# Performance work log

Measured on AMD Instinct MI355X. Metric: run time of the kernel, lower is better.

Reference implementation:

```python
import jax, jax.numpy as jnp
import numpy as np

B, C, H, W = 2, 64, 128, 128
O = 64
KH = KW = 3
KK = KH * KW
STRIDE, PAD, DIL = 1, 1, 1
DG = 1            # deformable groups
CG = C // DG      # channels per deformable group
Ho = (H + 2 * PAD - DIL * (KH - 1) - 1) // STRIDE + 1
Wo = (W + 2 * PAD - DIL * (KW - 1) - 1) // STRIDE + 1


def setup_inputs() -> dict:
    key = jax.random.key(0)
    k1, k2, k3, k4, k5, k6 = jax.random.split(key, 6)
    input_offset = jax.random.normal(k1, (B, C, H, W), jnp.float32)
    input_real = jax.random.normal(k2, (B, C, H, W), jnp.float32)
    # conv_offset_mask: out = DG*3*KK channels. (Zero-init in the module; use
    # small random weights so offsets are non-trivial but only a few pixels.)
    w_om = jax.random.normal(k3, (DG * 3 * KK, C, KH, KW), jnp.float32) * 0.02
    b_om = jax.random.normal(k4, (DG * 3 * KK,), jnp.float32) * 0.02
    # DCN weight (groups=1): (O, C, KH, KW)
    fan_in = C * KK
    w_dcn = jax.random.normal(k5, (O, C, KH, KW), jnp.float32) / np.sqrt(fan_in)
    b_dcn = jax.random.normal(k6, (O,), jnp.float32) * 0.01
    return {"input_offset": input_offset, "input_real": input_real,
            "w_om": w_om, "b_om": b_om, "w_dcn": w_dcn, "b_dcn": b_dcn}


def _modulated_deform_conv(x, offset, mask, w, b):
    # x: (B,C,H,W); offset: (B, DG*2*KK, Ho, Wo) interleaved (y,x) per kernel pt
    # mask: (B, DG*KK, Ho, Wo) already sigmoid'ed; w: (O,C,KH,KW); b: (O,)
    off = offset.reshape(B, DG, KK, 2, Ho, Wo)
    off_y, off_x = off[:, :, :, 0], off[:, :, :, 1]          # (B,DG,KK,Ho,Wo)
    m = mask.reshape(B, DG, KK, Ho, Wo)

    ky = jnp.repeat(jnp.arange(KH), KW).astype(jnp.float32)  # (KK,)
    kx = jnp.tile(jnp.arange(KW), KH).astype(jnp.float32)
    base_y = (ky[:, None, None] * DIL
              + jnp.arange(Ho, dtype=jnp.float32)[None, :, None] * STRIDE - PAD)
    base_x = (kx[:, None, None] * DIL
              + jnp.arange(Wo, dtype=jnp.float32)[None, None, :] * STRIDE - PAD)
    y = base_y[None, None] + off_y                           # (B,DG,KK,Ho,Wo)
    x_ = base_x[None, None] + off_x

    y0 = jnp.floor(y); x0 = jnp.floor(x_)
    ly = y - y0; lx = x_ - x0
    hy = 1.0 - ly; hx = 1.0 - lx

    xg = x.reshape(B, DG, CG, H * W)                         # grouped spatialflat

    def gather(iy, ix):
        valid = ((iy >= 0) & (iy < H) & (ix >= 0) & (ix < W)).astype(jnp.float32)
        iyc = jnp.clip(iy, 0, H - 1).astype(jnp.int32)
        ixc = jnp.clip(ix, 0, W - 1).astype(jnp.int32)
        idx = (iyc * W + ixc).reshape(B, DG, 1, KK * Ho * Wo)
        v = jnp.take_along_axis(xg, idx, axis=3)
        v = v.reshape(B, DG, CG, KK, Ho, Wo)
        return v * valid[:, :, None]

    val = (gather(y0,       x0      ) * (hy * hx)[:, :, None]
         + gather(y0,       x0 + 1.0) * (hy * lx)[:, :, None]
         + gather(y0 + 1.0, x0      ) * (ly * hx)[:, :, None]
         + gather(y0 + 1.0, x0 + 1.0) * (ly * lx)[:, :, None])
    val = val * m[:, :, None]                                # (B,DG,CG,KK,Ho,Wo)

    wr = w.reshape(O, DG, CG, KK)
    out = jnp.einsum('bdckhw,odck->bohw', val, wr) + b[None, :, None, None]
    return out


def reference(input_offset, input_real, w_om, b_om, w_dcn, b_dcn):
    # conv_offset_mask
    om = jax.lax.conv_general_dilated(
        input_offset, w_om, window_strides=(STRIDE, STRIDE),
        padding=((PAD, PAD), (PAD, PAD)),
        dimension_numbers=('NCHW', 'OIHW', 'NCHW'))
    om = om + b_om[None, :, None, None]
    n = DG * KK
    o1, o2, mraw = om[:, :n], om[:, n:2 * n], om[:, 2 * n:]
    offset = jnp.concatenate((o1, o2), axis=1)               # (B, 2*DG*KK, Ho, Wo)
    mask = jax.nn.sigmoid(mraw)                              # (B, DG*KK, Ho, Wo)
    out = _modulated_deform_conv(input_real, offset, mask, w_dcn, b_dcn)
    return out, offset
```

## Files before the change

### kernel.cpp

```cpp
#include <hip/hip_runtime.h>
#include <math.h>

constexpr int BB   = 2;
constexpr int CC   = 64;
constexpr int HH   = 128;
constexpr int WW   = 128;
constexpr int OO   = 64;
constexpr int HWSZ = HH * WW;
constexpr int HOWO = 16384;
constexpr int OMC  = 27;

typedef __attribute__((ext_vector_type(8))) short short8v;
typedef __attribute__((ext_vector_type(4))) float f32x4;
typedef unsigned short ushortT;

__device__ __forceinline__ ushortT f2bf(float x) {
    unsigned int u = __builtin_bit_cast(unsigned int, x);
    u = (u + 0x7FFFu + ((u >> 16) & 1u)) >> 16;
    return (ushortT)u;
}
__device__ __forceinline__ float bf2f(ushortT u) {
    return __builtin_bit_cast(float, (unsigned int)u << 16);
}

__global__ __launch_bounds__(256) void xtpose_prep(
    const float* __restrict__ xr, const float* __restrict__ xo,
    ushortT* __restrict__ xtr, ushortT* __restrict__ xto,
    const float* __restrict__ w_dcn, const float* __restrict__ w_om,
    ushortT* __restrict__ Wdswz, ushortT* __restrict__ Womswz)
{
    __shared__ float t[64][129];
    const int tid = threadIdx.x;
    const int bid = blockIdx.x;

    if (bid < 512) {
        const int by = bid & 255;
        const int b  = by >> 7, y = by & 127;
        const float* src = (bid < 256) ? xr : xo;
        ushortT*    dst  = (bid < 256) ? xtr : xto;

#pragma unroll
        for (int cc = 0; cc < 64; cc += 2) {
            const int c  = cc + (tid >> 7);
            const int xw = tid & 127;
            t[c][xw] = src[((size_t)(b * 64 + c) * 128 + y) * 128 + xw];
        }
        __syncthreads();

#pragma unroll
        for (int r = 0; r < 8; ++r) {
            const int idx = r * 256 + tid;
            const int xw  = idx >> 4;
            const int cq  = (idx & 15) << 2;
            ushort4 pk = make_ushort4(f2bf(t[cq][xw]), f2bf(t[cq + 1][xw]),
                                      f2bf(t[cq + 2][xw]), f2bf(t[cq + 3][xw]));
            *(ushort4*)(dst + (((size_t)by * 128 + xw) << 6) + cq) = pk;
        }
    } else {
        const int idx = (bid - 512) * 256 + tid;
        if (idx < 64 * 576) {
            const int j    = idx & 7;
            const int lane = (idx >> 3) & 63;
            const int ks   = (idx >> 9) % 18;
            const int wid  = idx / (8 * 64 * 18);
            const int l15  = lane & 15;
            const int l4   = lane >> 4;
            const int oc   = (wid << 4) + l15;
            const int k    = ks * 32 + l4 * 8 + j;
            const int kk   = k >> 6;
            const int c    = k & 63;
            Wdswz[idx] = f2bf(w_dcn[(oc * CC + c) * 9 + kk]);
        }
        if (idx < 32 * 576) {
            const int j    = idx & 7;
            const int lane = (idx >> 3) & 63;
            const int ks   = (idx >> 9) % 18;
            const int half = idx / (8 * 64 * 18);
            const int l15  = lane & 15;
            const int l4   = lane >> 4;
            const int oc   = (half << 4) + l15;
            const int k    = ks * 32 + l4 * 8 + j;
            const int kk   = k >> 6;
            const int c    = k & 63;
            Womswz[idx] = (oc < OMC) ? f2bf(w_om[(oc * CC + c) * 9 + kk])
                                     : (ushortT)0;
        }
    }
}

__device__ __forceinline__ void bilinear_params(
    float oy, float ox, float m, int ho, int wo, int ky, int kx,
    float& w00, float& w01, float& w10, float& w11,
    int& i00, int& i01, int& i10, int& i11)
{
    const float yf = (float)(ho + ky - 1) + oy;
    const float xf = (float)(wo + kx - 1) + ox;
    const float y0 = floorf(yf), x0 = floorf(xf);
    const float ly = yf - y0, lx = xf - x0;
    const float hy = 1.f - ly, hx = 1.f - lx;
    const int iy0 = (int)y0, ix0 = (int)x0;
    const int iy1 = iy0 + 1, ix1 = ix0 + 1;
    const bool vy0 = (unsigned)iy0 < (unsigned)HH;
    const bool vy1 = (unsigned)iy1 < (unsigned)HH;
    const bool vx0 = (unsigned)ix0 < (unsigned)WW;
    const bool vx1 = (unsigned)ix1 < (unsigned)WW;
    w00 = (vy0 && vx0) ? hy * hx * m : 0.f;
    w01 = (vy0 && vx1) ? hy * lx * m : 0.f;
    w10 = (vy1 && vx0) ? ly * hx * m : 0.f;
    w11 = (vy1 && vx1) ? ly * lx * m : 0.f;
    const int cy0 = min(max(iy0, 0), HH - 1), cy1 = min(max(iy1, 0), HH - 1);
    const int cx0 = min(max(ix0, 0), WW - 1), cx1 = min(max(ix1, 0), WW - 1);
    i00 = cy0 * WW + cx0; i01 = cy0 * WW + cx1;
    i10 = cy1 * WW + cx0; i11 = cy1 * WW + cx1;
}

__device__ __forceinline__ void gather_issue(
    const int s, const int tid, const int pl, const size_t bbase,
    const float (*offm)[28], const ushortT* __restrict__ xtr,
    short8v (&pay)[3][4], float (&gw)[3][4], int (&wadr)[3])
{
    const int ch0 = (tid & 7) << 3;
#pragma unroll
    for (int rr = 0; rr < 3; ++rr) {
        const int rnd  = s * 3 + rr;
        const int task = rnd * 32 + (tid >> 3);
        const int gpix = task & 63;
        const int kk   = task >> 6;
        const int pg   = pl + gpix;
        const int gho  = pg >> 7, gwo = pg & 127;
        const int ky   = kk / 3, kx = kk - 3 * ky;

        float w00, w01, w10, w11; int i00, i01, i10, i11;
        bilinear_params(offm[gpix][2 * kk], offm[gpix][2 * kk + 1],
                        offm[gpix][18 + kk], gho, gwo, ky, kx,
                        w00, w01, w10, w11, i00, i01, i10, i11);
        gw[rr][0] = w00; gw[rr][1] = w01; gw[rr][2] = w10; gw[rr][3] = w11;

        pay[rr][0] = *(const short8v*)(xtr + ((bbase + i00) << 6) + ch0);
        pay[rr][1] = *(const short8v*)(xtr + ((bbase + i01) << 6) + ch0);
        pay[rr][2] = *(const short8v*)(xtr + ((bbase + i10) << 6) + ch0);
        pay[rr][3] = *(const short8v*)(xtr + ((bbase + i11) << 6) + ch0);

        wadr[rr] = gpix * 1152 + ((((kk << 6) + ch0) << 1) ^ ((gpix & 7) << 4));
    }
}

__device__ __forceinline__ void gather_combine(
    ushortT* vlds, const short8v (&pay)[3][4], const float (&gw)[3][4],
    const int (&wadr)[3])
{
#pragma unroll
    for (int rr = 0; rr < 3; ++rr) {
        short8v pk;
#pragma unroll
        for (int j = 0; j < 8; ++j) {
            const float v = gw[rr][0] * bf2f((ushortT)pay[rr][0][j]) +
                            gw[rr][1] * bf2f((ushortT)pay[rr][1][j]) +
                            gw[rr][2] * bf2f((ushortT)pay[rr][2][j]) +
                            gw[rr][3] * bf2f((ushortT)pay[rr][3][j]);
            pk[j] = (short)f2bf(v);
        }
        *(short8v*)((char*)vlds + wadr[rr]) = pk;
    }
}

__global__ __launch_bounds__(256, 2) void fused_mlp(
    const ushortT* __restrict__ xtr,
    const ushortT* __restrict__ xto,
    const ushortT* __restrict__ Womswz,
    const float* __restrict__ bom,
    const ushortT* __restrict__ Wdswz,
    const float* __restrict__ bd,
    float* __restrict__ out,
    float* __restrict__ off_out)
{
    __shared__ ushortT vlds[64 * 576];
    __shared__ float offm[64][28];

    const int tid  = threadIdx.x;
    const int lane = tid & 63;
    const int wid  = tid >> 6;
    const int l15  = lane & 15;
    const int l4   = lane >> 4;
    const int p0   = blockIdx.x * 64;
    const int b    = p0 >> 14;
    const int pl   = p0 & 16383;
    const size_t bbase = (size_t)(b << 14);

    {
        const int lpix = (wid << 4) + l15;
        const int pix  = pl + lpix;
        const int ho   = pix >> 7, wo = pix & 127;

        short8v xv[18];
        unsigned int vmask = 0;
#pragma unroll
        for (int ks = 0; ks < 18; ++ks) {
            const int kk = ks >> 1;
            const int ky = kk / 3, kx = kk - 3 * ky;
            const int iy = ho + ky - 1, ix = wo + kx - 1;
            if (((unsigned)iy < 128u) && ((unsigned)ix < 128u)) vmask |= (1u << ks);
            const int cy = min(max(iy, 0), 127), cx = min(max(ix, 0), 127);
            const int c0 = ((ks & 1) << 5) + (l4 << 3);
            xv[ks] = *(const short8v*)(xto + ((bbase + cy * 128 + cx) << 6) + c0);
        }

        f32x4 acc0 = {0.f, 0.f, 0.f, 0.f};
        f32x4 acc1 = {0.f, 0.f, 0.f, 0.f};
        const short8v zero8 = {0, 0, 0, 0, 0, 0, 0, 0};
        const ushortT* womL = Womswz + (lane << 3);

#pragma unroll
        for (int ks = 0; ks < 18; ++ks) {
            const short8v bf = (vmask & (1u << ks)) ? xv[ks] : zero8;
            const short8v ah0 = *(const short8v*)(womL + (ks << 9));
            const short8v ah1 = *(const short8v*)(womL + ((18 + ks) << 9));
            acc0 = __builtin_amdgcn_mfma_f32_16x16x32_bf16(ah0, bf, acc0, 0, 0, 0);
            acc1 = __builtin_amdgcn_mfma_f32_16x16x32_bf16(ah1, bf, acc1, 0, 0, 0);
        }

#pragma unroll
        for (int r = 0; r < 4; ++r) {
            const int oca = (l4 << 2) + r;
            const float va = acc0[r] + bom[oca];
            offm[lpix][oca] = va;
            off_out[(b * 18 + oca) * HOWO + pix] = va;
            const int ocb = 16 + (l4 << 2) + r;
            if (ocb < 18) {
                const float vb = acc1[r] + bom[ocb];
                offm[lpix][ocb] = vb;
                off_out[(b * 18 + ocb) * HOWO + pix] = vb;
            } else if (ocb < OMC) {
                offm[lpix][ocb] = 1.f / (1.f + expf(-(acc1[r] + bom[ocb])));
            }
        }
    }
    __syncthreads();

    {
        short8v payA[3][4], payB[3][4];
        float gwA[3][4], gwB[3][4];
        int wA[3], wB[3];

        gather_issue(0, tid, pl, bbase, offm, xtr, payA, gwA, wA);
        gather_issue(1, tid, pl, bbase, offm, xtr, payB, gwB, wB);
        gather_combine(vlds, payA, gwA, wA);
        gather_issue(2, tid, pl, bbase, offm, xtr, payA, gwA, wA);
        gather_combine(vlds, payB, gwB, wB);
        gather_issue(3, tid, pl, bbase, offm, xtr, payB, gwB, wB);
        gather_combine(vlds, payA, gwA, wA);
        gather_issue(4, tid, pl, bbase, offm, xtr, payA, gwA, wA);
        gather_combine(vlds, payB, gwB, wB);
        gather_issue(5, tid, pl, bbase, offm, xtr, payB, gwB, wB);
        gather_combine(vlds, payA, gwA, wA);
        gather_combine(vlds, payB, gwB, wB);
    }
    __syncthreads();

    {
        const int oc0 = wid << 4;
        const ushortT* wdL = Wdswz + ((wid * 18) << 9) + (lane << 3);
        const int swz = (l15 & 7) << 4;
        const int kl  = l4 << 4;

        f32x4 ac0 = {0.f, 0.f, 0.f, 0.f};
        f32x4 ac1 = {0.f, 0.f, 0.f, 0.f};
        f32x4 ac2 = {0.f, 0.f, 0.f, 0.f};
        f32x4 ac3 = {0.f, 0.f, 0.f, 0.f};

#pragma unroll
        for (int ks = 0; ks < 18; ++ks) {
            const short8v ahi = *(const short8v*)(wdL + (ks << 9));
            const int inrow = ((ks << 6) + kl) ^ swz;
            const char* base = (const char*)vlds + inrow;
            const short8v b0 = *(const short8v*)(base + (l15 + 0)  * 1152);
            const short8v b1 = *(const short8v*)(base + (l15 + 16) * 1152);
            const short8v b2 = *(const short8v*)(base + (l15 + 32) * 1152);
            const short8v b3 = *(const short8v*)(base + (l15 + 48) * 1152);
            ac0 = __builtin_amdgcn_mfma_f32_16x16x32_bf16(ahi, b0, ac0, 0, 0, 0);
            ac1 = __builtin_amdgcn_mfma_f32_16x16x32_bf16(ahi, b1, ac1, 0, 0, 0);
            ac2 = __builtin_amdgcn_mfma_f32_16x16x32_bf16(ahi, b2, ac2, 0, 0, 0);
            ac3 = __builtin_amdgcn_mfma_f32_16x16x32_bf16(ahi, b3, ac3, 0, 0, 0);
        }

#pragma unroll
        for (int r = 0; r < 4; ++r) {
            const int oc = oc0 + (l4 << 2) + r;
            const float bias = bd[oc];
            const size_t ob = ((size_t)(b * OO + oc)) * HOWO + pl + l15;
            out[ob + 0]  = ac0[r] + bias;
            out[ob + 16] = ac1[r] + bias;
            out[ob + 32] = ac2[r] + bias;
            out[ob + 48] = ac3[r] + bias;
        }
    }
}

__global__ __launch_bounds__(256) void prep_transpose(
    const float* __restrict__ w_dcn, const float* __restrict__ w_om,
    float* __restrict__ wt_dcn, float* __restrict__ wt_om)
{
    int idx = blockIdx.x * 256 + threadIdx.x;
    if (idx < 9 * 64 * 64) {
        int o  = idx & 63;
        int c  = (idx >> 6) & 63;
        int kk = idx >> 12;
        wt_dcn[idx] = w_dcn[(o * CC + c) * 9 + kk];
    }
    if (idx < 9 * 64 * 28) {
        int o    = idx % 28;
        int rest = idx / 28;
        int c    = rest & 63;
        int kk   = rest >> 6;
        wt_om[idx] = (o < OMC) ? w_om[(o * CC + c) * 9 + kk] : 0.f;
    }
}

__global__ __launch_bounds__(256) void conv_om2(
    const float* __restrict__ x, const float* __restrict__ wtom,
    const float* __restrict__ bom, float* __restrict__ off_out,
    float* __restrict__ mask_out)
{
    const int pg  = blockIdx.x * 256 + threadIdx.x;
    const int b   = pg >> 14;
    const int p   = pg & 16383;
    const int ho  = p >> 7, wo = p & 127;
    const int oc0 = blockIdx.y << 3;

    float acc[8];
#pragma unroll
    for (int j = 0; j < 8; ++j) acc[j] = 0.f;

    const float* xb = x + (size_t)b * CC * HWSZ;
    for (int c = 0; c < CC; ++c) {
        const float* xc = xb + c * HWSZ;
        float t[9];
#pragma unroll
        for (int kh = 0; kh < 3; ++kh) {
            const int ih = ho + kh - 1;
            const bool rv = (unsigned)ih < (unsigned)HH;
#pragma unroll
            for (int kw = 0; kw < 3; ++kw) {
                const int iw = wo + kw - 1;
                t[kh * 3 + kw] =
                    (rv && (unsigned)iw < (unsigned)WW) ? xc[ih * WW + iw] : 0.f;
            }
        }
#pragma unroll
        for (int kk = 0; kk < 9; ++kk) {
            const float tv = t[kk];
            const float4* wr = (const float4*)(wtom + ((kk << 6) + c) * 28 + oc0);
            const float4 w0 = wr[0];
            const float4 w1 = wr[1];
            acc[0] += tv * w0.x; acc[1] += tv * w0.y;
            acc[2] += tv * w0.z; acc[3] += tv * w0.w;
            acc[4] += tv * w1.x; acc[5] += tv * w1.y;
            acc[6] += tv * w1.z; acc[7] += tv * w1.w;
        }
    }
#pragma unroll
    for (int j = 0; j < 8; ++j) {
        const int oc = oc0 + j;
        if (oc < 18) {
            off_out[(b * 18 + oc) * HOWO + p] = acc[j] + bom[oc];
        } else if (oc < OMC) {
            mask_out[(b * 9 + (oc - 18)) * HOWO + p] =
                1.f / (1.f + expf(-(acc[j] + bom[oc])));
        }
    }
}

__global__ __launch_bounds__(256) void dcn2(
    const float* __restrict__ xr, const float* __restrict__ off,
    const float* __restrict__ mask, const float* __restrict__ wtd,
    const float* __restrict__ bd, float* __restrict__ out)
{
    __shared__ float offm[32][29];
    __shared__ float vtile[64 * 33];

    const int tid  = threadIdx.x;
    const int pixl = tid & 31;
    const int grp  = tid >> 5;
    const int p0g  = blockIdx.x * 32;
    const int b    = p0g >> 14;
    const int p0   = p0g & 16383;
    const int p    = p0 + pixl;
    const int ho   = p >> 7, wo = p & 127;

    for (int it = tid; it < 32 * 27; it += 256) {
        const int pp = it & 31;
        const int o  = it >> 5;
        offm[pp][o] = (o < 18)
            ? off[(b * 18 + o) * HOWO + p0 + pp]
            : mask[(b * 9 + (o - 18)) * HOWO + p0 + pp];
    }
    __syncthreads();

    float acc[8];
#pragma unroll
    for (int j = 0; j < 8; ++j) acc[j] = 0.f;

    const float* xrb = xr + (size_t)b * CC * HWSZ;

    for (int kk = 0; kk < 9; ++kk) {
        {
            const int ky = kk / 3, kx = kk - ky * 3;
            float w00, w01, w10, w11; int i00, i01, i10, i11;
            bilinear_params(offm[pixl][2 * kk], offm[pixl][2 * kk + 1],
                            offm[pixl][18 + kk], ho, wo, ky, kx,
                            w00, w01, w10, w11, i00, i01, i10, i11);
            const float* xg = xrb + (grp << 3) * HWSZ;
#pragma unroll
            for (int i = 0; i < 8; ++i) {
                const float* xc = xg + i * HWSZ;
                const float v = w00 * xc[i00] + w01 * xc[i01] +
                                w10 * xc[i10] + w11 * xc[i11];
                vtile[((grp << 3) + i) * 33 + pixl] = v;
            }
        }
        __syncthreads();

        const float* wk = wtd + (kk << 12) + (grp << 3);
#pragma unroll 8
        for (int c = 0; c < 64; ++c) {
            const float v = vtile[c * 33 + pixl];
            const float4* wr = (const float4*)(wk + (c << 6));
            const float4 w0 = wr[0];
            const float4 w1 = wr[1];
            acc[0] += v * w0.x; acc[1] += v * w0.y;
            acc[2] += v * w0.z; acc[3] += v * w0.w;
            acc[4] += v * w1.x; acc[5] += v * w1.y;
            acc[6] += v * w1.z; acc[7] += v * w1.w;
        }
        __syncthreads();
    }

#pragma unroll
    for (int q = 0; q < 8; ++q) {
        const int oc = (grp << 3) + q;
        out[((size_t)(b * OO + oc)) * HOWO + p0 + pixl] = acc[q] + bd[oc];
    }
}

__global__ __launch_bounds__(256) void conv_om_slow(
    const float* __restrict__ x, const float* __restrict__ w,
    const float* __restrict__ bias, float* __restrict__ off_out)
{
    const int xid = blockIdx.x;
    const int b   = xid >> 6;
    const int p   = ((xid & 63) << 8) + threadIdx.x;
    const int ho  = p >> 7, wo = p & 127;
    const int oc0 = blockIdx.y << 4;

    float acc[16];
#pragma unroll
    for (int j = 0; j < 16; ++j) {
        const int oc = oc0 + j;
        acc[j] = (oc < OMC) ? bias[oc] : 0.f;
    }
    const float* xb = x + (size_t)b * CC * HWSZ;
    for (int c = 0; c < CC; ++c) {
        const float* xc = xb + c * HWSZ;
        float t[9];
#pragma unroll
        for (int kh = 0; kh < 3; ++kh) {
            const int ih = ho + kh - 1;
            const bool rv = (unsigned)ih < (unsigned)HH;
#pragma unroll
            for (int kw = 0; kw < 3; ++kw) {
                const int iw = wo + kw - 1;
                t[kh * 3 + kw] =
                    (rv && (unsigned)iw < (unsigned)WW) ? xc[ih * WW + iw] : 0.f;
            }
        }
#pragma unroll
        for (int j = 0; j < 16; ++j) {
            const int oc = oc0 + j;
            if (oc < OMC) {
                const float* wj = w + (size_t)(oc * CC + c) * 9;
                float s = 0.f;
#pragma unroll
                for (int kk = 0; kk < 9; ++kk) s += t[kk] * wj[kk];
                acc[j] += s;
            }
        }
    }
#pragma unroll
    for (int j = 0; j < 16; ++j) {
        const int oc = oc0 + j;
        if (oc < 18) off_out[(b * 18 + oc) * HOWO + p] = acc[j];
    }
}

__global__ __launch_bounds__(256) void dcn_slow(
    const float* __restrict__ xr, const float* __restrict__ off,
    const float* __restrict__ wd, const float* __restrict__ bd,
    float* __restrict__ out, const float* __restrict__ xo,
    const float* __restrict__ wom, const float* __restrict__ bom)
{
    const int xid = blockIdx.x;
    const int b   = xid >> 6;
    const int p   = ((xid & 63) << 8) + threadIdx.x;
    const int ho  = p >> 7, wo = p & 127;
    const int o0  = blockIdx.y << 4;

    float acc[16];
#pragma unroll
    for (int j = 0; j < 16; ++j) acc[j] = bd[o0 + j];
    const float* xb = xr + (size_t)b * CC * HWSZ;

    for (int kk = 0; kk < 9; ++kk) {
        const float oy = off[(b * 18 + 2 * kk) * HOWO + p];
        const float ox = off[(b * 18 + 2 * kk + 1) * HOWO + p];
        float a = bom[18 + kk];
        const float* xob = xo + (size_t)b * CC * HWSZ;
        for (int c = 0; c < CC; ++c) {
            const float* xc2 = xob + c * HWSZ;
            const float* wj  = wom + (size_t)((18 + kk) * CC + c) * 9;
#pragma unroll
            for (int kh = 0; kh < 3; ++kh) {
                const int ih = ho + kh - 1;
                if ((unsigned)ih < (unsigned)HH) {
#pragma unroll
                    for (int kw = 0; kw < 3; ++kw) {
                        const int iw = wo + kw - 1;
                        if ((unsigned)iw < (unsigned)WW)
                            a += xc2[ih * WW + iw] * wj[kh * 3 + kw];
                    }
                }
            }
        }
        const float m = 1.f / (1.f + expf(-a));
        const int ky = kk / 3, kx = kk - ky * 3;
        float w00, w01, w10, w11; int i00, i01, i10, i11;
        bilinear_params(oy, ox, m, ho, wo, ky, kx,
                        w00, w01, w10, w11, i00, i01, i10, i11);
#pragma unroll 4
        for (int c = 0; c < CC; ++c) {
            const float* xc = xb + c * HWSZ;
            const float v = w00 * xc[i00] + w01 * xc[i01] +
                            w10 * xc[i10] + w11 * xc[i11];
#pragma unroll
            for (int j = 0; j < 16; ++j)
                acc[j] += v * wd[(size_t)((o0 + j) * CC + c) * 9 + kk];
        }
    }
#pragma unroll
    for (int j = 0; j < 16; ++j)
        out[((size_t)b * OO + o0 + j) * HOWO + p] = acc[j];
}

extern "C" void kernel_launch(void* const* d_in, const int* in_sizes, int n_in,
                              void* d_out, int out_size, void* d_ws, size_t ws_size,
                              hipStream_t stream)
{
    const float* x_off  = (const float*)d_in[0];
    const float* x_real = (const float*)d_in[1];
    const float* w_om   = (const float*)d_in[2];
    const float* b_om   = (const float*)d_in[3];
    const float* w_dcn  = (const float*)d_in[4];
    const float* b_dcn  = (const float*)d_in[5];

    float* out = (float*)d_out;
    const int outElems = BB * OO * HOWO;
    float* off_out = out + outElems;

    const size_t xtB   = (size_t)BB * HWSZ * CC * 2;
    const size_t wdB   = (size_t)64 * 576 * 2;
    const size_t womB  = (size_t)32 * 576 * 2;
    const size_t need_full = 2 * xtB + wdB + womB;

    const size_t wtDcnF = 9 * 64 * 64;
    const size_t wtOmF  = 9 * 64 * 28;
    const size_t need_mid = (wtDcnF + wtOmF + (size_t)BB * 9 * HOWO) * 4;

    if (ws_size >= need_full) {
        char* w = (char*)d_ws;
        ushortT* xtr    = (ushortT*)w;   w += xtB;
        ushortT* xto    = (ushortT*)w;   w += xtB;
        ushortT* Wdswz  = (ushortT*)w;   w += wdB;
        ushortT* Womswz = (ushortT*)w;

        hipLaunchKernelGGL(xtpose_prep, dim3(656), dim3(256), 0, stream,
                           x_real, x_off, xtr, xto, w_dcn, w_om,
                           Wdswz, Womswz);
        hipLaunchKernelGGL(fused_mlp, dim3(512), dim3(256), 0, stream,
                           xtr, xto, Womswz, b_om, Wdswz, b_dcn,
                           out, off_out);
    } else if (ws_size >= need_mid) {
        float* wtDcn   = (float*)d_ws;
        float* wtOm    = wtDcn + wtDcnF;
        float* maskBuf = wtOm + wtOmF;
        hipLaunchKernelGGL(prep_transpose, dim3(144), dim3(256), 0, stream,
                           w_dcn, w_om, wtDcn, wtOm);
        hipLaunchKernelGGL(conv_om2, dim3(128, 4), dim3(256), 0, stream,
                           x_off, wtOm, b_om, off_out, maskBuf);
        hipLaunchKernelGGL(dcn2, dim3(1024), dim3(256), 0, stream,
                           x_real, off_out, maskBuf, wtDcn, b_dcn, out);
    } else {
        hipLaunchKernelGGL(conv_om_slow, dim3(128, 2), dim3(256), 0, stream,
                           x_off, w_om, b_om, off_out);
        hipLaunchKernelGGL(dcn_slow, dim3(128, 4), dim3(256), 0, stream,
                           x_real, off_out, w_dcn, b_dcn, out,
                           x_off, w_om, b_om);
    }
}
```

Measured before the change: 34.34 us.

## Halve pixel tile per block to 32 and split offset conv across wave pairs

The fused deformable-conv kernel now processes 32 output pixels per block instead of 64, doubling the grid to 1024 blocks and halving LDS use so three blocks per CU can be resident. In the offset conv, each pair of waves now splits the 27 offset/mask channels (one MFMA chain per wave) instead of each wave computing both halves. The gather and final GEMM phases are resized to match. The aim is more blocks in flight to hide gather latency, at the cost of reloading weights for every smaller block and duplicating the input-offset loads across wave pairs.

Result: slower. 40.32 us (+17.4%).

```diff
diff --git a/kernel.cpp b/kernel.cpp
--- a/kernel.cpp
+++ b/kernel.cpp
@@ -114,7 +114,7 @@
     i10 = cy1 * WW + cx0; i11 = cy1 * WW + cx1;
 }
 
-__device__ __forceinline__ void gather_issue(
+__device__ __forceinline__ void gather_issue32(
     const int s, const int tid, const int pl, const size_t bbase,
     const float (*offm)[28], const ushortT* __restrict__ xtr,
     short8v (&pay)[3][4], float (&gw)[3][4], int (&wadr)[3])
@@ -124,8 +124,8 @@
     for (int rr = 0; rr < 3; ++rr) {
         const int rnd  = s * 3 + rr;
         const int task = rnd * 32 + (tid >> 3);
-        const int gpix = task & 63;
-        const int kk   = task >> 6;
+        const int gpix = task & 31;
+        const int kk   = task >> 5;
         const int pg   = pl + gpix;
         const int gho  = pg >> 7, gwo = pg & 127;
         const int ky   = kk / 3, kx = kk - 3 * ky;
@@ -145,7 +145,7 @@
     }
 }
 
-__device__ __forceinline__ void gather_combine(
+__device__ __forceinline__ void gather_combine32(
     ushortT* vlds, const short8v (&pay)[3][4], const float (&gw)[3][4],
     const int (&wadr)[3])
 {
@@ -164,7 +164,7 @@
     }
 }
 
-__global__ __launch_bounds__(256, 2) void fused_mlp(
+__global__ __launch_bounds__(256, 3) void fused32(
     const ushortT* __restrict__ xtr,
     const ushortT* __restrict__ xto,
     const ushortT* __restrict__ Womswz,
@@ -174,21 +174,23 @@
     float* __restrict__ out,
     float* __restrict__ off_out)
 {
-    __shared__ ushortT vlds[64 * 576];
-    __shared__ float offm[64][28];
+    __shared__ ushortT vlds[32 * 576];
+    __shared__ float offm[32][28];
 
     const int tid  = threadIdx.x;
     const int lane = tid & 63;
     const int wid  = tid >> 6;
     const int l15  = lane & 15;
     const int l4   = lane >> 4;
-    const int p0   = blockIdx.x * 64;
+    const int p0   = blockIdx.x * 32;
     const int b    = p0 >> 14;
     const int pl   = p0 & 16383;
     const size_t bbase = (size_t)(b << 14);
 
     {
-        const int lpix = (wid << 4) + l15;
+        const int q = wid >> 1;
+        const int h = wid & 1;
+        const int lpix = (h << 4) + l15;
         const int pix  = pl + lpix;
         const int ho   = pix >> 7, wo = pix & 127;
 
@@ -205,33 +207,26 @@
             xv[ks] = *(const short8v*)(xto + ((bbase + cy * 128 + cx) << 6) + c0);
         }
 
-        f32x4 acc0 = {0.f, 0.f, 0.f, 0.f};
-        f32x4 acc1 = {0.f, 0.f, 0.f, 0.f};
+        f32x4 acc = {0.f, 0.f, 0.f, 0.f};
         const short8v zero8 = {0, 0, 0, 0, 0, 0, 0, 0};
-        const ushortT* womL = Womswz + (lane << 3);
+        const ushortT* womL = Womswz + ((q * 18) << 9) + (lane << 3);
 
 #pragma unroll
         for (int ks = 0; ks < 18; ++ks) {
             const short8v bf = (vmask & (1u << ks)) ? xv[ks] : zero8;
-            const short8v ah0 = *(const short8v*)(womL + (ks << 9));
-            const short8v ah1 = *(const short8v*)(womL + ((18 + ks) << 9));
-            acc0 = __builtin_amdgcn_mfma_f32_16x16x32_bf16(ah0, bf, acc0, 0, 0, 0);
-            acc1 = __builtin_amdgcn_mfma_f32_16x16x32_bf16(ah1, bf, acc1, 0, 0, 0);
+            const short8v ah = *(const short8v*)(womL + (ks << 9));
+            acc = __builtin_amdgcn_mfma_f32_16x16x32_bf16(ah, bf, acc, 0, 0, 0);
         }
 
 #pragma unroll
         for (int r = 0; r < 4; ++r) {
-            const int oca = (l4 << 2) + r;
-            const float va = acc0[r] + bom[oca];
-            offm[lpix][oca] = va;
-            off_out[(b * 18 + oca) * HOWO + pix] = va;
-            const int ocb = 16 + (l4 << 2) + r;
-            if (ocb < 18) {
-                const float vb = acc1[r] + bom[ocb];
-                offm[lpix][ocb] = vb;
-                off_out[(b * 18 + ocb) * HOWO + pix] = vb;
-            } else if (ocb < OMC) {
-                offm[lpix][ocb] = 1.f / (1.f + expf(-(acc1[r] + bom[ocb])));
+            const int oc = (q << 4) + (l4 << 2) + r;
+            if (oc < 18) {
+                const float v = acc[r] + bom[oc];
+                offm[lpix][oc] = v;
+                off_out[(b * 18 + oc) * HOWO + pix] = v;
+            } else if (oc < OMC) {
+                offm[lpix][oc] = 1.f / (1.f + expf(-(acc[r] + bom[oc])));
             }
         }
     }
@@ -242,18 +237,12 @@
         float gwA[3][4], gwB[3][4];
         int wA[3], wB[3];
 
-        gather_issue(0, tid, pl, bbase, offm, xtr, payA, gwA, wA);
-        gather_issue(1, tid, pl, bbase, offm, xtr, payB, gwB, wB);
-        gather_combine(vlds, payA, gwA, wA);
-        gather_issue(2, tid, pl, bbase, offm, xtr, payA, gwA, wA);
-        gather_combine(vlds, payB, gwB, wB);
-        gather_issue(3, tid, pl, bbase, offm, xtr, payB, gwB, wB);
-        gather_combine(vlds, payA, gwA, wA);
-        gather_issue(4, tid, pl, bbase, offm, xtr, payA, gwA, wA);
-        gather_combine(vlds, payB, gwB, wB);
-        gather_issue(5, tid, pl, bbase, offm, xtr, payB, gwB, wB);
-        gather_combine(vlds, payA, gwA, wA);
-        gather_combine(vlds, payB, gwB, wB);
+        gather_issue32(0, tid, pl, bbase, offm, xtr, payA, gwA, wA);
+        gather_issue32(1, tid, pl, bbase, offm, xtr, payB, gwB, wB);
+        gather_combine32(vlds, payA, gwA, wA);
+        gather_issue32(2, tid, pl, bbase, offm, xtr, payA, gwA, wA);
+        gather_combine32(vlds, payB, gwB, wB);
+        gather_combine32(vlds, payA, gwA, wA);
     }
     __syncthreads();
 
@@ -265,8 +254,6 @@
 
         f32x4 ac0 = {0.f, 0.f, 0.f, 0.f};
         f32x4 ac1 = {0.f, 0.f, 0.f, 0.f};
-        f32x4 ac2 = {0.f, 0.f, 0.f, 0.f};
-        f32x4 ac3 = {0.f, 0.f, 0.f, 0.f};
 
 #pragma unroll
         for (int ks = 0; ks < 18; ++ks) {
@@ -275,12 +262,8 @@
             const char* base = (const char*)vlds + inrow;
             const short8v b0 = *(const short8v*)(base + (l15 + 0)  * 1152);
             const short8v b1 = *(const short8v*)(base + (l15 + 16) * 1152);
-            const short8v b2 = *(const short8v*)(base + (l15 + 32) * 1152);
-            const short8v b3 = *(const short8v*)(base + (l15 + 48) * 1152);
             ac0 = __builtin_amdgcn_mfma_f32_16x16x32_bf16(ahi, b0, ac0, 0, 0, 0);
             ac1 = __builtin_amdgcn_mfma_f32_16x16x32_bf16(ahi, b1, ac1, 0, 0, 0);
-            ac2 = __builtin_amdgcn_mfma_f32_16x16x32_bf16(ahi, b2, ac2, 0, 0, 0);
-            ac3 = __builtin_amdgcn_mfma_f32_16x16x32_bf16(ahi, b3, ac3, 0, 0, 0);
         }
 
 #pragma unroll
@@ -290,8 +273,6 @@
             const size_t ob = ((size_t)(b * OO + oc)) * HOWO + pl + l15;
             out[ob + 0]  = ac0[r] + bias;
             out[ob + 16] = ac1[r] + bias;
-            out[ob + 32] = ac2[r] + bias;
-            out[ob + 48] = ac3[r] + bias;
         }
     }
 }
@@ -584,7 +565,7 @@
         hipLaunchKernelGGL(xtpose_prep, dim3(656), dim3(256), 0, stream,
                            x_real, x_off, xtr, xto, w_dcn, w_om,
                            Wdswz, Womswz);
-        hipLaunchKernelGGL(fused_mlp, dim3(512), dim3(256), 0, stream,
+        hipLaunchKernelGGL(fused32, dim3(1024), dim3(256), 0, stream,
                            xtr, xto, Womswz, b_om, Wdswz, b_dcn,
                            out, off_out);
     } else if (ws_size >= need_mid) {
```
